# Kernel optimization log

Hardware: AMD Instinct MI355X
Metric: run time of the kernel (lower is better)

## Reference

```python
import jax, jax.numpy as jnp
import numpy as np

D = 1024
HS = 64
NH = D // HS
NEG_INF = -1e30


def setup_inputs() -> dict:
    key = jax.random.key(0)
    ks = jax.random.split(key, 8)
    B, S = 4, 2048
    x = jax.random.normal(ks[0], (B, S, D), dtype=jnp.float32)
    y = jax.random.normal(ks[1], (B, S, D), dtype=jnp.float32)
    pad_mask = jnp.ones((B, S), dtype=jnp.int32)
    time_attention = jnp.ones((S, S), dtype=jnp.int32)
    scale = 1.0 / np.sqrt(D)
    Wq = jax.random.normal(ks[2], (D, D), dtype=jnp.float32) * scale
    Wk = jax.random.normal(ks[3], (D, D), dtype=jnp.float32) * scale
    Wv = jax.random.normal(ks[4], (D, D), dtype=jnp.float32) * scale
    Wp = jax.random.normal(ks[5], (D, D), dtype=jnp.float32) * scale
    bp = jnp.zeros((D,), dtype=jnp.float32)
    return {"x": x, "y": y, "pad_mask": pad_mask, "time_attention": time_attention,
            "Wq": Wq, "Wk": Wk, "Wv": Wv, "Wp": Wp, "bp": bp}


def reference(x, y, pad_mask, time_attention, Wq, Wk, Wv, Wp, bp):
    B, S, _ = x.shape
    Sy = y.shape[1]
    # q/k/v projections (Linear: x @ W.T), split into heads -> [B, H, S, hs]
    q = (y @ Wq.T).reshape(B, Sy, NH, HS).transpose(0, 2, 1, 3)
    k = (x @ Wk.T).reshape(B, S, NH, HS).transpose(0, 2, 1, 3)
    v = (x @ Wv.T).reshape(B, S, NH, HS).transpose(0, 2, 1, 3)
    # scaled scores [B, H, Sy, S]
    att = jnp.einsum('bhqe,bhke->bhqk', q, k) * (HS ** -0.5)
    # causal mask (tril[:S, :S])
    causal = jnp.tril(jnp.ones((S, S), dtype=jnp.bool_))
    att = jnp.where(causal[None, None, :Sy, :], att, NEG_INF)
    # pad mask over kv positions
    att = jnp.where(pad_mask[:, None, None, :] != 0, att, NEG_INF)
    # time attention mask [Sq, Sk]
    att = jnp.where(time_attention[None, None, :Sy, :] != 0, att, NEG_INF)
    p = jax.nn.softmax(att, axis=-1)  # dropout p=0 -> identity
    out = jnp.einsum('bhqk,bhke->bhqe', p, v)
    out = out.transpose(0, 2, 1, 3).reshape(B, Sy, D)
    return out @ Wp.T + bp
```

## Files before the change

kernel.cpp:

```cpp
#include <hip/hip_runtime.h>
#include <hip/hip_bf16.h>
#include <stdint.h>
#include <stddef.h>


typedef __attribute__((ext_vector_type(4))) float f32x4;
typedef __attribute__((ext_vector_type(8))) short s16x8;
typedef __attribute__((ext_vector_type(4))) float float4v;
typedef __attribute__((ext_vector_type(4))) int i32x4;
typedef __attribute__((ext_vector_type(2))) unsigned int u32x2;

#define DEV __device__ __forceinline__

constexpr int Bsz = 4, Sseq = 2048, Dm = 1024, NHn = 16, HSn = 64;
constexpr float QSCALE = 0.125f * 1.4426950408889634f;

constexpr size_t SZ_BF_XY = (size_t)Bsz * Sseq * Dm * 2;
constexpr size_t SZ_W     = (size_t)Dm * Dm * 2;
constexpr size_t OFF_XBF  = 0;
constexpr size_t OFF_YBF  = OFF_XBF + SZ_BF_XY;
constexpr size_t OFF_WQ   = OFF_YBF + SZ_BF_XY;
constexpr size_t OFF_WK   = OFF_WQ + SZ_W;
constexpr size_t OFF_WV   = OFF_WK + SZ_W;
constexpr size_t OFF_WP   = OFF_WV + SZ_W;
constexpr size_t OFF_QWS  = OFF_WP + SZ_W;
constexpr size_t OFF_KWS  = OFF_QWS + SZ_BF_XY;
constexpr size_t OFF_VTWS = OFF_KWS + SZ_BF_XY;
constexpr size_t OFF_OWS  = OFF_VTWS + SZ_BF_XY;
constexpr size_t OFF_FLAG = OFF_OWS + SZ_BF_XY;

DEV unsigned short f2bf(float f) {
  union { float f; unsigned int u; } v; v.f = f;
  unsigned int r = (v.u + 0x7FFFu + ((v.u >> 16) & 1u)) >> 16;
  return (unsigned short)r;
}

DEV void gll16(const void* g, void* l) {
  __builtin_amdgcn_global_load_lds((const __attribute__((address_space(1))) unsigned int*)g,
                                   (__attribute__((address_space(3))) unsigned int*)l, 16, 0, 0);
}

DEV unsigned int cvtpk(float a, float b) {
  unsigned int r;
  asm("v_cvt_pk_bf16_f32 %0, %1, %2" : "=v"(r) : "v"(a), "v"(b));
  return r;
}

__global__ void cvt_all(const float* __restrict__ x, const float* __restrict__ y,
                        const float* __restrict__ Wq, const float* __restrict__ Wk,
                        const float* __restrict__ Wv, const float* __restrict__ Wp,
                        const int* __restrict__ pad, const int* __restrict__ tmask,
                        char* __restrict__ ws, int* __restrict__ flags) {
  const int blk = blockIdx.x;
  if (blk >= 10240) {
    int bad = 0;
    if (blk < 10248) {
      const i32x4 v = ((const i32x4*)pad)[(blk - 10240) * 256 + threadIdx.x];
      bad = (v[0] == 0) | (v[1] == 0) | (v[2] == 0) | (v[3] == 0);
    } else {
      const i32x4* tp = (const i32x4*)tmask + ((size_t)(blk - 10248) * 256 + threadIdx.x) * 2;
      i32x4 v0 = tp[0], v1 = tp[1];
      bad = (v0[0] == 0) | (v0[1] == 0) | (v0[2] == 0) | (v0[3] == 0) |
            (v1[0] == 0) | (v1[1] == 0) | (v1[2] == 0) | (v1[3] == 0);
    }
    if (__builtin_amdgcn_ballot_w64(bad) != 0 && (threadIdx.x & 63) == 0)
      atomicOr(flags, 1);
    return;
  }
  const float* src;
  unsigned short* dst;
  int b8;
  float scale = 1.f;
  if (blk < 4096)      { src = x;  dst = (unsigned short*)(ws + OFF_XBF); b8 = blk; }
  else if (blk < 8192) { src = y;  dst = (unsigned short*)(ws + OFF_YBF); b8 = blk - 4096; }
  else if (blk < 8704) { src = Wq; dst = (unsigned short*)(ws + OFF_WQ);  b8 = blk - 8192; scale = QSCALE; }
  else if (blk < 9216) { src = Wk; dst = (unsigned short*)(ws + OFF_WK);  b8 = blk - 8704; }
  else if (blk < 9728) { src = Wv; dst = (unsigned short*)(ws + OFF_WV);  b8 = blk - 9216; }
  else                 { src = Wp; dst = (unsigned short*)(ws + OFF_WP);  b8 = blk - 9728; }
  const size_t i = (size_t)b8 * 256 + threadIdx.x;
  const float4v* s = (const float4v*)src + i * 2;
  float4v a = s[0], b = s[1];
  s16x8 o;
  o[0] = (short)f2bf(a[0] * scale); o[1] = (short)f2bf(a[1] * scale);
  o[2] = (short)f2bf(a[2] * scale); o[3] = (short)f2bf(a[3] * scale);
  o[4] = (short)f2bf(b[0] * scale); o[5] = (short)f2bf(b[1] * scale);
  o[6] = (short)f2bf(b[2] * scale); o[7] = (short)f2bf(b[3] * scale);
  *(s16x8*)(dst + i * 8) = o;
}

__global__ __launch_bounds__(256) void q_gemm(const unsigned short* __restrict__ A,
                                              const unsigned short* __restrict__ W,
                                              unsigned short* __restrict__ outb) {
  constexpr int K = 1024;
  __shared__ unsigned short sm[8192];
  unsigned short* lA = sm;
  unsigned short* lB = sm + 4096;
  const int tid = threadIdx.x;
  const int w = tid >> 6, lane = tid & 63, lo = lane & 15, hi = lane >> 4;
  const int wm = w >> 1, wn = w & 1;
  const int m0 = blockIdx.x * 128, n0 = blockIdx.y * 128;
  f32x4 acc[4][4] = {};

  for (int k0 = 0; k0 < K; k0 += 32) {
#pragma unroll
    for (int h = 0; h < 2; ++h) {
      int c = w * 64 + h * 256 + lane;
      gll16(A + (size_t)(m0 + (c >> 2)) * K + k0 + (c & 3) * 8, lA + (size_t)(w * 64 + h * 256) * 8);
      gll16(W + (size_t)(n0 + (c >> 2)) * K + k0 + (c & 3) * 8, lB + (size_t)(w * 64 + h * 256) * 8);
    }
    __syncthreads();
    s16x8 af[4], bfr[4];
#pragma unroll
    for (int mi = 0; mi < 4; ++mi) af[mi] = *(const s16x8*)&lA[(wm * 64 + mi * 16 + lo) * 32 + hi * 8];
#pragma unroll
    for (int ni = 0; ni < 4; ++ni) bfr[ni] = *(const s16x8*)&lB[(wn * 64 + ni * 16 + lo) * 32 + hi * 8];
#pragma unroll
    for (int mi = 0; mi < 4; ++mi)
#pragma unroll
      for (int ni = 0; ni < 4; ++ni)
        acc[mi][ni] = __builtin_amdgcn_mfma_f32_16x16x32_bf16(af[mi], bfr[ni], acc[mi][ni], 0, 0, 0);
    __syncthreads();
  }
#pragma unroll
  for (int mi = 0; mi < 4; ++mi)
#pragma unroll
    for (int ni = 0; ni < 4; ++ni)
#pragma unroll
      for (int j = 0; j < 4; ++j) {
        int m = m0 + wm * 64 + mi * 16 + hi * 4 + j;
        int n = n0 + wn * 64 + ni * 16 + lo;
        int b = m >> 11, s = m & 2047, hh = n >> 6, e = n & 63;
        outb[((size_t)(b * NHn + hh) * Sseq + s) * HSn + e] = f2bf(acc[mi][ni][j]);
      }
}

__global__ __launch_bounds__(256, 2) void kv_gemm(const unsigned short* __restrict__ A,
                                                  const unsigned short* __restrict__ Wk,
                                                  const unsigned short* __restrict__ Wv,
                                                  unsigned short* __restrict__ kws,
                                                  unsigned short* __restrict__ vtw) {
  constexpr int K = 1024;
  __shared__ unsigned short sm[17408];
  unsigned short* lA = sm;
  unsigned short* lBk = sm + 4096;
  unsigned short* lBv = sm + 8192;
  const int tid = threadIdx.x;
  const int w = tid >> 6, lane = tid & 63, lo = lane & 15, hi = lane >> 4;
  const int wm = w >> 1, wn = w & 1;
  const int m0 = blockIdx.x * 128, n0 = blockIdx.y * 128;
  f32x4 acck[4][4] = {}, accv[4][4] = {};

  for (int k0 = 0; k0 < K; k0 += 32) {
#pragma unroll
    for (int h = 0; h < 2; ++h) {
      int c = w * 64 + h * 256 + lane;
      size_t roff = (size_t)(c >> 2) * K + k0 + (c & 3) * 8;
      size_t loff = (size_t)(w * 64 + h * 256) * 8;
      gll16(A + (size_t)m0 * K + roff, lA + loff);
      gll16(Wk + (size_t)n0 * K + roff, lBk + loff);
      gll16(Wv + (size_t)n0 * K + roff, lBv + loff);
    }
    __syncthreads();
    s16x8 af[4], bfk[4], bfv[4];
#pragma unroll
    for (int mi = 0; mi < 4; ++mi) af[mi] = *(const s16x8*)&lA[(wm * 64 + mi * 16 + lo) * 32 + hi * 8];
#pragma unroll
    for (int ni = 0; ni < 4; ++ni) {
      bfk[ni] = *(const s16x8*)&lBk[(wn * 64 + ni * 16 + lo) * 32 + hi * 8];
      bfv[ni] = *(const s16x8*)&lBv[(wn * 64 + ni * 16 + lo) * 32 + hi * 8];
    }
#pragma unroll
    for (int mi = 0; mi < 4; ++mi)
#pragma unroll
      for (int ni = 0; ni < 4; ++ni) {
        acck[mi][ni] = __builtin_amdgcn_mfma_f32_16x16x32_bf16(af[mi], bfk[ni], acck[mi][ni], 0, 0, 0);
        accv[mi][ni] = __builtin_amdgcn_mfma_f32_16x16x32_bf16(af[mi], bfv[ni], accv[mi][ni], 0, 0, 0);
      }
    __syncthreads();
  }

#pragma unroll
  for (int mi = 0; mi < 4; ++mi)
#pragma unroll
    for (int ni = 0; ni < 4; ++ni)
#pragma unroll
      for (int j = 0; j < 4; ++j) {
        int m = m0 + wm * 64 + mi * 16 + hi * 4 + j;
        int n = n0 + wn * 64 + ni * 16 + lo;
        int b = m >> 11, s = m & 2047, hh = n >> 6, e = n & 63;
        kws[((size_t)(b * NHn + hh) * Sseq + s) * HSn + e] = f2bf(acck[mi][ni][j]);
      }
  __syncthreads();
#pragma unroll
  for (int mi = 0; mi < 4; ++mi)
#pragma unroll
    for (int ni = 0; ni < 4; ++ni)
#pragma unroll
      for (int j = 0; j < 4; ++j) {
        int ml = wm * 64 + mi * 16 + hi * 4 + j;
        int nl = wn * 64 + ni * 16 + lo;
        sm[(size_t)nl * 136 + ml] = f2bf(accv[mi][ni][j]);
      }
  __syncthreads();
  int nl = tid >> 1, half = tid & 1;
  int b = m0 >> 11, hh = (n0 + nl) >> 6, e = (n0 + nl) & 63;
  unsigned short* dst = vtw + ((size_t)(b * NHn + hh) * HSn + e) * Sseq + (m0 & 2047) + half * 64;
#pragma unroll
  for (int i = 0; i < 8; ++i)
    *(s16x8*)(dst + i * 8) = *(const s16x8*)&sm[(size_t)nl * 136 + half * 64 + i * 8];
}

__global__ __launch_bounds__(256) void gemm_p(const unsigned short* __restrict__ A,
                                              const unsigned short* __restrict__ W,
                                              float* __restrict__ outf,
                                              const float* __restrict__ bias) {
  constexpr int K = 1024;
  __shared__ unsigned short sm[8192];
  unsigned short* lA = sm;
  unsigned short* lB = sm + 4096;
  const int tid = threadIdx.x;
  const int w = tid >> 6, lane = tid & 63, lo = lane & 15, hi = lane >> 4;
  const int wm = w >> 1, wn = w & 1;
  const int m0 = blockIdx.x * 128, n0 = blockIdx.y * 128;
  f32x4 acc[4][4] = {};
  for (int k0 = 0; k0 < K; k0 += 32) {
#pragma unroll
    for (int h = 0; h < 2; ++h) {
      int c = w * 64 + h * 256 + lane;
      gll16(A + (size_t)(m0 + (c >> 2)) * K + k0 + (c & 3) * 8, lA + (size_t)(w * 64 + h * 256) * 8);
      gll16(W + (size_t)(n0 + (c >> 2)) * K + k0 + (c & 3) * 8, lB + (size_t)(w * 64 + h * 256) * 8);
    }
    __syncthreads();
    s16x8 af[4], bfr[4];
#pragma unroll
    for (int mi = 0; mi < 4; ++mi) af[mi] = *(const s16x8*)&lA[(wm * 64 + mi * 16 + lo) * 32 + hi * 8];
#pragma unroll
    for (int ni = 0; ni < 4; ++ni) bfr[ni] = *(const s16x8*)&lB[(wn * 64 + ni * 16 + lo) * 32 + hi * 8];
#pragma unroll
    for (int mi = 0; mi < 4; ++mi)
#pragma unroll
      for (int ni = 0; ni < 4; ++ni)
        acc[mi][ni] = __builtin_amdgcn_mfma_f32_16x16x32_bf16(af[mi], bfr[ni], acc[mi][ni], 0, 0, 0);
    __syncthreads();
  }
  float bv[4];
#pragma unroll
  for (int ni = 0; ni < 4; ++ni) bv[ni] = bias[n0 + wn * 64 + ni * 16 + lo];
#pragma unroll
  for (int mi = 0; mi < 4; ++mi)
#pragma unroll
    for (int ni = 0; ni < 4; ++ni)
#pragma unroll
      for (int j = 0; j < 4; ++j) {
        int m = m0 + wm * 64 + mi * 16 + hi * 4 + j;
        int n = n0 + wn * 64 + ni * 16 + lo;
        outf[(size_t)m * 1024 + n] = acc[mi][ni][j] + bv[ni];
      }
}

DEV void attn_unit16(const unsigned short* __restrict__ kbc,
                     const unsigned short* __restrict__ vbc,
                     const s16x8 (&qf)[2], f32x4 (&oacc)[4], f32x4& lacc,
                     float& mrun, const s16x8& ones,
                     unsigned short* __restrict__ pbw,
                     int k0, int qw0, int lo, int hi, int b,
                     const int* __restrict__ pad, const int* __restrict__ tmask,
                     bool trivial) {
  if (k0 > qw0 + 15) return;

  f32x4 st[4];
#pragma unroll
  for (int t = 0; t < 4; ++t) {
    f32x4 z = {0.f, 0.f, 0.f, 0.f};
#pragma unroll
    for (int kk = 0; kk < 2; ++kk) {
      s16x8 kfr = *(const s16x8*)&kbc[(t * 16 + lo) * 72 + kk * 32 + hi * 8];
      z = __builtin_amdgcn_mfma_f32_16x16x32_bf16(kfr, qf[kk], z, 0, 0, 0);
    }
    st[t] = z;
  }
  const int qg = qw0 + lo;
  if (k0 + 63 > qw0) {
#pragma unroll
    for (int t = 0; t < 4; ++t)
#pragma unroll
      for (int j = 0; j < 4; ++j)
        if (k0 + t * 16 + hi * 4 + j > qg) st[t][j] = -3e38f;
  }
  if (!trivial) {
#pragma unroll
    for (int t = 0; t < 4; ++t)
#pragma unroll
      for (int j = 0; j < 4; ++j) {
        int kg = k0 + t * 16 + hi * 4 + j;
        if (!pad[b * Sseq + kg] || !tmask[(size_t)qg * Sseq + kg]) st[t][j] = -3e38f;
      }
  }
  float m0v = fmaxf(fmaxf(st[0][0], st[0][1]), fmaxf(st[0][2], st[0][3]));
  float m1v = fmaxf(fmaxf(st[1][0], st[1][1]), fmaxf(st[1][2], st[1][3]));
  float m2v = fmaxf(fmaxf(st[2][0], st[2][1]), fmaxf(st[2][2], st[2][3]));
  float m3v = fmaxf(fmaxf(st[3][0], st[3][1]), fmaxf(st[3][2], st[3][3]));
  float mx = fmaxf(fmaxf(m0v, m1v), fmaxf(m2v, m3v));
  mx = fmaxf(mx, __shfl_xor(mx, 16, 64));
  mx = fmaxf(mx, __shfl_xor(mx, 32, 64));
  if (!__all(mx <= mrun + 11.f)) {
    const float mnew = fmaxf(mrun, mx);
    const float al = __builtin_amdgcn_exp2f(mrun - mnew);
    mrun = mnew;
#pragma unroll
    for (int et = 0; et < 4; ++et) oacc[et] *= al;
    lacc *= al;
  }
#pragma unroll
  for (int t = 0; t < 4; ++t)
#pragma unroll
    for (int j = 0; j < 4; ++j)
      st[t][j] = __builtin_amdgcn_exp2f(st[t][j] - mrun);
#pragma unroll
  for (int t = 0; t < 4; ++t) {
    u32x2 dd = {cvtpk(st[t][0], st[t][1]), cvtpk(st[t][2], st[t][3])};
    *(u32x2*)&pbw[lo * 72 + t * 16 + hi * 4] = dd;
  }
  s16x8 pf[2];
#pragma unroll
  for (int kk = 0; kk < 2; ++kk)
    pf[kk] = *(const s16x8*)&pbw[lo * 72 + kk * 32 + hi * 8];
#pragma unroll
  for (int et = 0; et < 4; ++et)
#pragma unroll
    for (int kk = 0; kk < 2; ++kk) {
      s16x8 vfr = *(const s16x8*)&vbc[(et * 16 + lo) * 72 + kk * 32 + hi * 8];
      oacc[et] = __builtin_amdgcn_mfma_f32_16x16x32_bf16(vfr, pf[kk], oacc[et], 0, 0, 0);
    }
  lacc = __builtin_amdgcn_mfma_f32_16x16x32_bf16(ones, pf[0], lacc, 0, 0, 0);
  lacc = __builtin_amdgcn_mfma_f32_16x16x32_bf16(ones, pf[1], lacc, 0, 0, 0);
}

DEV void attn_epi16(f32x4 (&oacc)[4], float lrun,
                    unsigned short* __restrict__ pbw,
                    unsigned short* __restrict__ O, int b, int hh, int qw0,
                    int lane, int lo, int hi) {
  const float inv = 1.f / lrun;
#pragma unroll
  for (int et = 0; et < 4; ++et) {
    f32x4 o = oacc[et] * inv;
    u32x2 d = {cvtpk(o[0], o[1]), cvtpk(o[2], o[3])};
    *(u32x2*)&pbw[lo * 72 + et * 16 + hi * 4] = d;
  }
  int q = lane >> 2, seg = lane & 3;
  unsigned short* dst = O + ((size_t)b * Sseq + qw0 + q) * Dm + hh * HSn + seg * 16;
  *(s16x8*)dst = *(const s16x8*)&pbw[q * 72 + seg * 16];
  *(s16x8*)(dst + 8) = *(const s16x8*)&pbw[q * 72 + seg * 16 + 8];
}

__global__ __launch_bounds__(512, 4) void attn_kernel(const unsigned short* __restrict__ Q,
                                                      const unsigned short* __restrict__ Kg,
                                                      const unsigned short* __restrict__ Vt,
                                                      unsigned short* __restrict__ O,
                                                      const int* __restrict__ pad,
                                                      const int* __restrict__ tmask,
                                                      const int* __restrict__ flags) {
  __shared__ unsigned short kb[2][64 * 72];
  __shared__ unsigned short vb[2][64 * 72];
  __shared__ unsigned short pb[8][16 * 72];

  const int ip = blockIdx.x, bh = blockIdx.y;
  const int b = bh >> 4, hh = bh & 15;
  const int tid = threadIdx.x, w = tid >> 6, lane = tid & 63, lo = lane & 15, hi = lane >> 4;
  const int qtA = ip, qtB = 15 - ip;
  const int qw0A = qtA * 128 + w * 16, qw0B = qtB * 128 + w * 16;
  const int ktA = 2 * qtA + 1;
  const int ktmax = 2 * qtB + 2;
  const bool trivial = flags[0] == 0;

  const unsigned short* Qb = Q + (size_t)bh * Sseq * HSn;
  const unsigned short* Kb = Kg + (size_t)bh * Sseq * HSn;
  const unsigned short* Vb = Vt + (size_t)bh * HSn * Sseq;

  s16x8 qfA[2], qfB[2];
#pragma unroll
  for (int kk = 0; kk < 2; ++kk) {
    qfA[kk] = *(const s16x8*)&Qb[(size_t)(qw0A + lo) * HSn + kk * 32 + hi * 8];
    qfB[kk] = *(const s16x8*)&Qb[(size_t)(qw0B + lo) * HSn + kk * 32 + hi * 8];
  }

  s16x8 ones;
#pragma unroll
  for (int j = 0; j < 8; ++j) ones[j] = (short)0x3F80;

  f32x4 oaccA[4] = {}, oaccB[4] = {};
  f32x4 laccA = {}, laccB = {};
  float mrunA = -3e38f, mrunB = -3e38f;

  const int shalf = tid >> 8, st_t = tid & 255;
  const int sr = st_t >> 2, sc = (st_t & 3) * 16;

  s16x8 r0, r1;
  if (shalf == 0) {
    const unsigned short* gk = Kb + (size_t)sr * HSn + sc;
    r0 = *(const s16x8*)gk; r1 = *(const s16x8*)(gk + 8);
    *(s16x8*)&kb[0][sr * 72 + sc] = r0; *(s16x8*)&kb[0][sr * 72 + sc + 8] = r1;
  } else {
    const unsigned short* gv = Vb + (size_t)sr * Sseq + sc;
    r0 = *(const s16x8*)gv; r1 = *(const s16x8*)(gv + 8);
    *(s16x8*)&vb[0][sr * 72 + sc] = r0; *(s16x8*)&vb[0][sr * 72 + sc + 8] = r1;
  }
  __syncthreads();

  for (int kt = 0; kt < ktmax; ++kt) {
    const int cur = kt & 1, k0 = kt * 64;
    const bool pre = (kt + 1 < ktmax);
    if (pre) {
      const int k1 = k0 + 64;
      if (shalf == 0) {
        const unsigned short* gk = Kb + (size_t)(k1 + sr) * HSn + sc;
        r0 = *(const s16x8*)gk; r1 = *(const s16x8*)(gk + 8);
      } else {
        const unsigned short* gv = Vb + (size_t)sr * Sseq + k1 + sc;
        r0 = *(const s16x8*)gv; r1 = *(const s16x8*)(gv + 8);
      }
    }
    const unsigned short* kbc = kb[cur];
    const unsigned short* vbc = vb[cur];
    if (kt <= ktA)
      attn_unit16(kbc, vbc, qfA, oaccA, laccA, mrunA, ones, pb[w],
                  k0, qw0A, lo, hi, b, pad, tmask, trivial);
    attn_unit16(kbc, vbc, qfB, oaccB, laccB, mrunB, ones, pb[w],
                k0, qw0B, lo, hi, b, pad, tmask, trivial);
    if (pre) {
      const int nb = cur ^ 1;
      if (shalf == 0) {
        *(s16x8*)&kb[nb][sr * 72 + sc] = r0; *(s16x8*)&kb[nb][sr * 72 + sc + 8] = r1;
      } else {
        *(s16x8*)&vb[nb][sr * 72 + sc] = r0; *(s16x8*)&vb[nb][sr * 72 + sc + 8] = r1;
      }
    }
    __syncthreads();
  }

  attn_epi16(oaccA, laccA[0], pb[w], O, b, hh, qw0A, lane, lo, hi);
  attn_epi16(oaccB, laccB[0], pb[w], O, b, hh, qw0B, lane, lo, hi);
}

extern "C" void kernel_launch(void* const* d_in, const int* in_sizes, int n_in,
                              void* d_out, int out_size, void* d_ws, size_t ws_size,
                              hipStream_t stream) {
  const float* x = (const float*)d_in[0];
  const float* y = (const float*)d_in[1];
  const int* pad = (const int*)d_in[2];
  const int* tmask = (const int*)d_in[3];
  const float* Wq = (const float*)d_in[4];
  const float* Wk = (const float*)d_in[5];
  const float* Wv = (const float*)d_in[6];
  const float* Wp = (const float*)d_in[7];
  const float* bp = (const float*)d_in[8];

  char* ws = (char*)d_ws;
  unsigned short* xbf = (unsigned short*)(ws + OFF_XBF);
  unsigned short* ybf = (unsigned short*)(ws + OFF_YBF);
  unsigned short* wqb = (unsigned short*)(ws + OFF_WQ);
  unsigned short* wkb = (unsigned short*)(ws + OFF_WK);
  unsigned short* wvb = (unsigned short*)(ws + OFF_WV);
  unsigned short* wpb = (unsigned short*)(ws + OFF_WP);
  unsigned short* qws = (unsigned short*)(ws + OFF_QWS);
  unsigned short* kws = (unsigned short*)(ws + OFF_KWS);
  unsigned short* vtw = (unsigned short*)(ws + OFF_VTWS);
  unsigned short* ows = (unsigned short*)(ws + OFF_OWS);
  int* flags = (int*)(ws + OFF_FLAG);

  hipMemsetAsync(flags, 0, 4, stream);
  cvt_all<<<12296, 256, 0, stream>>>(x, y, Wq, Wk, Wv, Wp, pad, tmask, ws, flags);

  q_gemm<<<dim3(64, 8), 256, 0, stream>>>(ybf, wqb, qws);
  kv_gemm<<<dim3(64, 8), 256, 0, stream>>>(xbf, wkb, wvb, kws, vtw);

  attn_kernel<<<dim3(8, 64), 512, 0, stream>>>(qws, kws, vtw, ows, pad, tmask, flags);

  gemm_p<<<dim3(64, 8), 256, 0, stream>>>(ows, wpb, (float*)d_out, bp);
}
```

Measured before the change: 192.8 us.

## Double-buffer GEMM LDS tiles and interleave attention A/B query units

The three projection GEMMs now use two LDS buffers. The loads for the next K-slice are issued before computing on the current one, so each iteration keeps one barrier instead of two and loads overlap with compute. In the attention kernel the two query tiles (A and B) are processed together per KV tile, so each K and V fragment is read from LDS once for both. This also gives the scheduler independent MFMA chains to interleave, and each warp gets separate P buffers for the two tiles. The costs are more LDS per block, which may lower occupancy, and a reliance on async LDS loads being complete at the single barrier.

```diff
diff --git a/kernel.cpp b/kernel.cpp
--- a/kernel.cpp
+++ b/kernel.cpp
@@ -92,23 +92,28 @@
                                               const unsigned short* __restrict__ W,
                                               unsigned short* __restrict__ outb) {
   constexpr int K = 1024;
-  __shared__ unsigned short sm[8192];
-  unsigned short* lA = sm;
-  unsigned short* lB = sm + 4096;
+  __shared__ unsigned short sm[2][8192];
   const int tid = threadIdx.x;
   const int w = tid >> 6, lane = tid & 63, lo = lane & 15, hi = lane >> 4;
   const int wm = w >> 1, wn = w & 1;
   const int m0 = blockIdx.x * 128, n0 = blockIdx.y * 128;
   f32x4 acc[4][4] = {};
 
-  for (int k0 = 0; k0 < K; k0 += 32) {
+  auto stage = [&](int buf, int k0) {
 #pragma unroll
     for (int h = 0; h < 2; ++h) {
       int c = w * 64 + h * 256 + lane;
-      gll16(A + (size_t)(m0 + (c >> 2)) * K + k0 + (c & 3) * 8, lA + (size_t)(w * 64 + h * 256) * 8);
-      gll16(W + (size_t)(n0 + (c >> 2)) * K + k0 + (c & 3) * 8, lB + (size_t)(w * 64 + h * 256) * 8);
-    }
-    __syncthreads();
+      gll16(A + (size_t)(m0 + (c >> 2)) * K + k0 + (c & 3) * 8, &sm[buf][0] + (size_t)(w * 64 + h * 256) * 8);
+      gll16(W + (size_t)(n0 + (c >> 2)) * K + k0 + (c & 3) * 8, &sm[buf][4096] + (size_t)(w * 64 + h * 256) * 8);
+    }
+  };
+
+  stage(0, 0);
+  __syncthreads();
+  for (int t = 0; t < 32; ++t) {
+    if (t < 31) stage((t + 1) & 1, (t + 1) * 32);
+    const unsigned short* lA = &sm[t & 1][0];
+    const unsigned short* lB = &sm[t & 1][4096];
     s16x8 af[4], bfr[4];
 #pragma unroll
     for (int mi = 0; mi < 4; ++mi) af[mi] = *(const s16x8*)&lA[(wm * 64 + mi * 16 + lo) * 32 + hi * 8];
@@ -140,27 +145,32 @@
                                                   unsigned short* __restrict__ kws,
                                                   unsigned short* __restrict__ vtw) {
   constexpr int K = 1024;
-  __shared__ unsigned short sm[17408];
-  unsigned short* lA = sm;
-  unsigned short* lBk = sm + 4096;
-  unsigned short* lBv = sm + 8192;
+  __shared__ unsigned short sm[2][12288];
   const int tid = threadIdx.x;
   const int w = tid >> 6, lane = tid & 63, lo = lane & 15, hi = lane >> 4;
   const int wm = w >> 1, wn = w & 1;
   const int m0 = blockIdx.x * 128, n0 = blockIdx.y * 128;
   f32x4 acck[4][4] = {}, accv[4][4] = {};
 
-  for (int k0 = 0; k0 < K; k0 += 32) {
+  auto stage = [&](int buf, int k0) {
 #pragma unroll
     for (int h = 0; h < 2; ++h) {
       int c = w * 64 + h * 256 + lane;
       size_t roff = (size_t)(c >> 2) * K + k0 + (c & 3) * 8;
       size_t loff = (size_t)(w * 64 + h * 256) * 8;
-      gll16(A + (size_t)m0 * K + roff, lA + loff);
-      gll16(Wk + (size_t)n0 * K + roff, lBk + loff);
-      gll16(Wv + (size_t)n0 * K + roff, lBv + loff);
-    }
-    __syncthreads();
+      gll16(A + (size_t)m0 * K + roff, &sm[buf][0] + loff);
+      gll16(Wk + (size_t)n0 * K + roff, &sm[buf][4096] + loff);
+      gll16(Wv + (size_t)n0 * K + roff, &sm[buf][8192] + loff);
+    }
+  };
+
+  stage(0, 0);
+  __syncthreads();
+  for (int t = 0; t < 32; ++t) {
+    if (t < 31) stage((t + 1) & 1, (t + 1) * 32);
+    const unsigned short* lA = &sm[t & 1][0];
+    const unsigned short* lBk = &sm[t & 1][4096];
+    const unsigned short* lBv = &sm[t & 1][8192];
     s16x8 af[4], bfk[4], bfv[4];
 #pragma unroll
     for (int mi = 0; mi < 4; ++mi) af[mi] = *(const s16x8*)&lA[(wm * 64 + mi * 16 + lo) * 32 + hi * 8];
@@ -190,6 +200,7 @@
         int b = m >> 11, s = m & 2047, hh = n >> 6, e = n & 63;
         kws[((size_t)(b * NHn + hh) * Sseq + s) * HSn + e] = f2bf(acck[mi][ni][j]);
       }
+  unsigned short* tp = &sm[0][0];
   __syncthreads();
 #pragma unroll
   for (int mi = 0; mi < 4; ++mi)
@@ -199,7 +210,7 @@
       for (int j = 0; j < 4; ++j) {
         int ml = wm * 64 + mi * 16 + hi * 4 + j;
         int nl = wn * 64 + ni * 16 + lo;
-        sm[(size_t)nl * 136 + ml] = f2bf(accv[mi][ni][j]);
+        tp[(size_t)nl * 136 + ml] = f2bf(accv[mi][ni][j]);
       }
   __syncthreads();
   int nl = tid >> 1, half = tid & 1;
@@ -207,7 +218,7 @@
   unsigned short* dst = vtw + ((size_t)(b * NHn + hh) * HSn + e) * Sseq + (m0 & 2047) + half * 64;
 #pragma unroll
   for (int i = 0; i < 8; ++i)
-    *(s16x8*)(dst + i * 8) = *(const s16x8*)&sm[(size_t)nl * 136 + half * 64 + i * 8];
+    *(s16x8*)(dst + i * 8) = *(const s16x8*)&tp[(size_t)nl * 136 + half * 64 + i * 8];
 }
 
 __global__ __launch_bounds__(256) void gemm_p(const unsigned short* __restrict__ A,
@@ -215,22 +226,28 @@
                                               float* __restrict__ outf,
                                               const float* __restrict__ bias) {
   constexpr int K = 1024;
-  __shared__ unsigned short sm[8192];
-  unsigned short* lA = sm;
-  unsigned short* lB = sm + 4096;
+  __shared__ unsigned short sm[2][8192];
   const int tid = threadIdx.x;
   const int w = tid >> 6, lane = tid & 63, lo = lane & 15, hi = lane >> 4;
   const int wm = w >> 1, wn = w & 1;
   const int m0 = blockIdx.x * 128, n0 = blockIdx.y * 128;
   f32x4 acc[4][4] = {};
-  for (int k0 = 0; k0 < K; k0 += 32) {
+
+  auto stage = [&](int buf, int k0) {
 #pragma unroll
     for (int h = 0; h < 2; ++h) {
       int c = w * 64 + h * 256 + lane;
-      gll16(A + (size_t)(m0 + (c >> 2)) * K + k0 + (c & 3) * 8, lA + (size_t)(w * 64 + h * 256) * 8);
-      gll16(W + (size_t)(n0 + (c >> 2)) * K + k0 + (c & 3) * 8, lB + (size_t)(w * 64 + h * 256) * 8);
-    }
-    __syncthreads();
+      gll16(A + (size_t)(m0 + (c >> 2)) * K + k0 + (c & 3) * 8, &sm[buf][0] + (size_t)(w * 64 + h * 256) * 8);
+      gll16(W + (size_t)(n0 + (c >> 2)) * K + k0 + (c & 3) * 8, &sm[buf][4096] + (size_t)(w * 64 + h * 256) * 8);
+    }
+  };
+
+  stage(0, 0);
+  __syncthreads();
+  for (int t = 0; t < 32; ++t) {
+    if (t < 31) stage((t + 1) & 1, (t + 1) * 32);
+    const unsigned short* lA = &sm[t & 1][0];
+    const unsigned short* lB = &sm[t & 1][4096];
     s16x8 af[4], bfr[4];
 #pragma unroll
     for (int mi = 0; mi < 4; ++mi) af[mi] = *(const s16x8*)&lA[(wm * 64 + mi * 16 + lo) * 32 + hi * 8];
@@ -258,27 +275,10 @@
       }
 }
 
-DEV void attn_unit16(const unsigned short* __restrict__ kbc,
-                     const unsigned short* __restrict__ vbc,
-                     const s16x8 (&qf)[2], f32x4 (&oacc)[4], f32x4& lacc,
-                     float& mrun, const s16x8& ones,
-                     unsigned short* __restrict__ pbw,
-                     int k0, int qw0, int lo, int hi, int b,
+DEV void softmax_col(f32x4 (&st)[4], int k0, int qw0, int lo, int hi, int b,
                      const int* __restrict__ pad, const int* __restrict__ tmask,
-                     bool trivial) {
-  if (k0 > qw0 + 15) return;
-
-  f32x4 st[4];
-#pragma unroll
-  for (int t = 0; t < 4; ++t) {
-    f32x4 z = {0.f, 0.f, 0.f, 0.f};
-#pragma unroll
-    for (int kk = 0; kk < 2; ++kk) {
-      s16x8 kfr = *(const s16x8*)&kbc[(t * 16 + lo) * 72 + kk * 32 + hi * 8];
-      z = __builtin_amdgcn_mfma_f32_16x16x32_bf16(kfr, qf[kk], z, 0, 0, 0);
-    }
-    st[t] = z;
-  }
+                     bool trivial, float& mrun, f32x4 (&oacc)[4], f32x4& lacc,
+                     unsigned short* __restrict__ pbw) {
   const int qg = qw0 + lo;
   if (k0 + 63 > qw0) {
 #pragma unroll
@@ -321,19 +321,6 @@
     u32x2 dd = {cvtpk(st[t][0], st[t][1]), cvtpk(st[t][2], st[t][3])};
     *(u32x2*)&pbw[lo * 72 + t * 16 + hi * 4] = dd;
   }
-  s16x8 pf[2];
-#pragma unroll
-  for (int kk = 0; kk < 2; ++kk)
-    pf[kk] = *(const s16x8*)&pbw[lo * 72 + kk * 32 + hi * 8];
-#pragma unroll
-  for (int et = 0; et < 4; ++et)
-#pragma unroll
-    for (int kk = 0; kk < 2; ++kk) {
-      s16x8 vfr = *(const s16x8*)&vbc[(et * 16 + lo) * 72 + kk * 32 + hi * 8];
-      oacc[et] = __builtin_amdgcn_mfma_f32_16x16x32_bf16(vfr, pf[kk], oacc[et], 0, 0, 0);
-    }
-  lacc = __builtin_amdgcn_mfma_f32_16x16x32_bf16(ones, pf[0], lacc, 0, 0, 0);
-  lacc = __builtin_amdgcn_mfma_f32_16x16x32_bf16(ones, pf[1], lacc, 0, 0, 0);
 }
 
 DEV void attn_epi16(f32x4 (&oacc)[4], float lrun,
@@ -362,14 +349,13 @@
                                                       const int* __restrict__ flags) {
   __shared__ unsigned short kb[2][64 * 72];
   __shared__ unsigned short vb[2][64 * 72];
-  __shared__ unsigned short pb[8][16 * 72];
+  __shared__ unsigned short pb[8][2][16 * 72];
 
   const int ip = blockIdx.x, bh = blockIdx.y;
   const int b = bh >> 4, hh = bh & 15;
   const int tid = threadIdx.x, w = tid >> 6, lane = tid & 63, lo = lane & 15, hi = lane >> 4;
   const int qtA = ip, qtB = 15 - ip;
   const int qw0A = qtA * 128 + w * 16, qw0B = qtB * 128 + w * 16;
-  const int ktA = 2 * qtA + 1;
   const int ktmax = 2 * qtB + 2;
   const bool trivial = flags[0] == 0;
 
@@ -422,11 +408,45 @@
     }
     const unsigned short* kbc = kb[cur];
     const unsigned short* vbc = vb[cur];
-    if (kt <= ktA)
-      attn_unit16(kbc, vbc, qfA, oaccA, laccA, mrunA, ones, pb[w],
-                  k0, qw0A, lo, hi, b, pad, tmask, trivial);
-    attn_unit16(kbc, vbc, qfB, oaccB, laccB, mrunB, ones, pb[w],
-                k0, qw0B, lo, hi, b, pad, tmask, trivial);
+    const bool actB = (k0 <= qw0B + 15);
+    if (actB) {
+      const bool actA = (k0 <= qw0A + 15);
+      f32x4 stA[4], stB[4];
+#pragma unroll
+      for (int t = 0; t < 4; ++t) {
+        f32x4 zA = {0.f, 0.f, 0.f, 0.f}, zB = {0.f, 0.f, 0.f, 0.f};
+#pragma unroll
+        for (int kk = 0; kk < 2; ++kk) {
+          s16x8 kfr = *(const s16x8*)&kbc[(t * 16 + lo) * 72 + kk * 32 + hi * 8];
+          if (actA) zA = __builtin_amdgcn_mfma_f32_16x16x32_bf16(kfr, qfA[kk], zA, 0, 0, 0);
+          zB = __builtin_amdgcn_mfma_f32_16x16x32_bf16(kfr, qfB[kk], zB, 0, 0, 0);
+        }
+        stA[t] = zA; stB[t] = zB;
+      }
+      if (actA)
+        softmax_col(stA, k0, qw0A, lo, hi, b, pad, tmask, trivial, mrunA, oaccA, laccA, pb[w][0]);
+      softmax_col(stB, k0, qw0B, lo, hi, b, pad, tmask, trivial, mrunB, oaccB, laccB, pb[w][1]);
+      s16x8 pfA[2], pfB[2];
+#pragma unroll
+      for (int kk = 0; kk < 2; ++kk) {
+        if (actA) pfA[kk] = *(const s16x8*)&pb[w][0][lo * 72 + kk * 32 + hi * 8];
+        pfB[kk] = *(const s16x8*)&pb[w][1][lo * 72 + kk * 32 + hi * 8];
+      }
+#pragma unroll
+      for (int et = 0; et < 4; ++et)
+#pragma unroll
+        for (int kk = 0; kk < 2; ++kk) {
+          s16x8 vfr = *(const s16x8*)&vbc[(et * 16 + lo) * 72 + kk * 32 + hi * 8];
+          if (actA) oaccA[et] = __builtin_amdgcn_mfma_f32_16x16x32_bf16(vfr, pfA[kk], oaccA[et], 0, 0, 0);
+          oaccB[et] = __builtin_amdgcn_mfma_f32_16x16x32_bf16(vfr, pfB[kk], oaccB[et], 0, 0, 0);
+        }
+      if (actA) {
+        laccA = __builtin_amdgcn_mfma_f32_16x16x32_bf16(ones, pfA[0], laccA, 0, 0, 0);
+        laccA = __builtin_amdgcn_mfma_f32_16x16x32_bf16(ones, pfA[1], laccA, 0, 0, 0);
+      }
+      laccB = __builtin_amdgcn_mfma_f32_16x16x32_bf16(ones, pfB[0], laccB, 0, 0, 0);
+      laccB = __builtin_amdgcn_mfma_f32_16x16x32_bf16(ones, pfB[1], laccB, 0, 0, 0);
+    }
     if (pre) {
       const int nb = cur ^ 1;
       if (shalf == 0) {
@@ -438,8 +458,8 @@
     __syncthreads();
   }
 
-  attn_epi16(oaccA, laccA[0], pb[w], O, b, hh, qw0A, lane, lo, hi);
-  attn_epi16(oaccB, laccB[0], pb[w], O, b, hh, qw0B, lane, lo, hi);
+  attn_epi16(oaccA, laccA[0], pb[w][0], O, b, hh, qw0A, lane, lo, hi);
+  attn_epi16(oaccB, laccB[0], pb[w][1], O, b, hh, qw0B, lane, lo, hi);
 }
 
 extern "C" void kernel_launch(void* const* d_in, const int* in_sizes, int n_in,
```

After: 212.6 us, median of 2. 1.1x slower.

## Double-buffer LDS tiles in projection GEMMs and swap attention grid order

Applied to the files above, without the earlier changes.

The three projection GEMMs now keep two LDS stages and issue the global-to-LDS loads for the next K-slice before computing on the current one, so memory latency can overlap with MFMA work. The attention launch swaps grid axes so that neighbouring blocks cover different heads and batches rather than query tiles of the same head, which changes dispatch order and load balance. The cost is double the LDS footprint per GEMM block, which can lower occupancy, especially in kv_gemm. The loop body visible here has no barrier between issuing the next stage and reading the current one, so correctness depends on the unseen tail of the loop keeping its trailing sync.

```diff
diff --git a/kernel.cpp b/kernel.cpp
--- a/kernel.cpp
+++ b/kernel.cpp
@@ -92,23 +92,28 @@
                                               const unsigned short* __restrict__ W,
                                               unsigned short* __restrict__ outb) {
   constexpr int K = 1024;
-  __shared__ unsigned short sm[8192];
-  unsigned short* lA = sm;
-  unsigned short* lB = sm + 4096;
+  __shared__ unsigned short sm[2][8192];
   const int tid = threadIdx.x;
   const int w = tid >> 6, lane = tid & 63, lo = lane & 15, hi = lane >> 4;
   const int wm = w >> 1, wn = w & 1;
   const int m0 = blockIdx.x * 128, n0 = blockIdx.y * 128;
   f32x4 acc[4][4] = {};
 
-  for (int k0 = 0; k0 < K; k0 += 32) {
+  auto stage = [&](int buf, int k0) {
 #pragma unroll
     for (int h = 0; h < 2; ++h) {
       int c = w * 64 + h * 256 + lane;
-      gll16(A + (size_t)(m0 + (c >> 2)) * K + k0 + (c & 3) * 8, lA + (size_t)(w * 64 + h * 256) * 8);
-      gll16(W + (size_t)(n0 + (c >> 2)) * K + k0 + (c & 3) * 8, lB + (size_t)(w * 64 + h * 256) * 8);
-    }
-    __syncthreads();
+      gll16(A + (size_t)(m0 + (c >> 2)) * K + k0 + (c & 3) * 8, &sm[buf][0] + (size_t)(w * 64 + h * 256) * 8);
+      gll16(W + (size_t)(n0 + (c >> 2)) * K + k0 + (c & 3) * 8, &sm[buf][4096] + (size_t)(w * 64 + h * 256) * 8);
+    }
+  };
+
+  stage(0, 0);
+  __syncthreads();
+  for (int t = 0; t < 32; ++t) {
+    if (t < 31) stage((t + 1) & 1, (t + 1) * 32);
+    const unsigned short* lA = &sm[t & 1][0];
+    const unsigned short* lB = &sm[t & 1][4096];
     s16x8 af[4], bfr[4];
 #pragma unroll
     for (int mi = 0; mi < 4; ++mi) af[mi] = *(const s16x8*)&lA[(wm * 64 + mi * 16 + lo) * 32 + hi * 8];
@@ -140,27 +145,32 @@
                                                   unsigned short* __restrict__ kws,
                                                   unsigned short* __restrict__ vtw) {
   constexpr int K = 1024;
-  __shared__ unsigned short sm[17408];
-  unsigned short* lA = sm;
-  unsigned short* lBk = sm + 4096;
-  unsigned short* lBv = sm + 8192;
+  __shared__ unsigned short sm[2][12288];
   const int tid = threadIdx.x;
   const int w = tid >> 6, lane = tid & 63, lo = lane & 15, hi = lane >> 4;
   const int wm = w >> 1, wn = w & 1;
   const int m0 = blockIdx.x * 128, n0 = blockIdx.y * 128;
   f32x4 acck[4][4] = {}, accv[4][4] = {};
 
-  for (int k0 = 0; k0 < K; k0 += 32) {
+  auto stage = [&](int buf, int k0) {
 #pragma unroll
     for (int h = 0; h < 2; ++h) {
       int c = w * 64 + h * 256 + lane;
       size_t roff = (size_t)(c >> 2) * K + k0 + (c & 3) * 8;
       size_t loff = (size_t)(w * 64 + h * 256) * 8;
-      gll16(A + (size_t)m0 * K + roff, lA + loff);
-      gll16(Wk + (size_t)n0 * K + roff, lBk + loff);
-      gll16(Wv + (size_t)n0 * K + roff, lBv + loff);
-    }
-    __syncthreads();
+      gll16(A + (size_t)m0 * K + roff, &sm[buf][0] + loff);
+      gll16(Wk + (size_t)n0 * K + roff, &sm[buf][4096] + loff);
+      gll16(Wv + (size_t)n0 * K + roff, &sm[buf][8192] + loff);
+    }
+  };
+
+  stage(0, 0);
+  __syncthreads();
+  for (int t = 0; t < 32; ++t) {
+    if (t < 31) stage((t + 1) & 1, (t + 1) * 32);
+    const unsigned short* lA = &sm[t & 1][0];
+    const unsigned short* lBk = &sm[t & 1][4096];
+    const unsigned short* lBv = &sm[t & 1][8192];
     s16x8 af[4], bfk[4], bfv[4];
 #pragma unroll
     for (int mi = 0; mi < 4; ++mi) af[mi] = *(const s16x8*)&lA[(wm * 64 + mi * 16 + lo) * 32 + hi * 8];
@@ -190,6 +200,7 @@
         int b = m >> 11, s = m & 2047, hh = n >> 6, e = n & 63;
         kws[((size_t)(b * NHn + hh) * Sseq + s) * HSn + e] = f2bf(acck[mi][ni][j]);
       }
+  unsigned short* tp = &sm[0][0];
   __syncthreads();
 #pragma unroll
   for (int mi = 0; mi < 4; ++mi)
@@ -199,7 +210,7 @@
       for (int j = 0; j < 4; ++j) {
         int ml = wm * 64 + mi * 16 + hi * 4 + j;
         int nl = wn * 64 + ni * 16 + lo;
-        sm[(size_t)nl * 136 + ml] = f2bf(accv[mi][ni][j]);
+        tp[(size_t)nl * 136 + ml] = f2bf(accv[mi][ni][j]);
       }
   __syncthreads();
   int nl = tid >> 1, half = tid & 1;
@@ -207,7 +218,7 @@
   unsigned short* dst = vtw + ((size_t)(b * NHn + hh) * HSn + e) * Sseq + (m0 & 2047) + half * 64;
 #pragma unroll
   for (int i = 0; i < 8; ++i)
-    *(s16x8*)(dst + i * 8) = *(const s16x8*)&sm[(size_t)nl * 136 + half * 64 + i * 8];
+    *(s16x8*)(dst + i * 8) = *(const s16x8*)&tp[(size_t)nl * 136 + half * 64 + i * 8];
 }
 
 __global__ __launch_bounds__(256) void gemm_p(const unsigned short* __restrict__ A,
@@ -215,22 +226,28 @@
                                               float* __restrict__ outf,
                                               const float* __restrict__ bias) {
   constexpr int K = 1024;
-  __shared__ unsigned short sm[8192];
-  unsigned short* lA = sm;
-  unsigned short* lB = sm + 4096;
+  __shared__ unsigned short sm[2][8192];
   const int tid = threadIdx.x;
   const int w = tid >> 6, lane = tid & 63, lo = lane & 15, hi = lane >> 4;
   const int wm = w >> 1, wn = w & 1;
   const int m0 = blockIdx.x * 128, n0 = blockIdx.y * 128;
   f32x4 acc[4][4] = {};
-  for (int k0 = 0; k0 < K; k0 += 32) {
+
+  auto stage = [&](int buf, int k0) {
 #pragma unroll
     for (int h = 0; h < 2; ++h) {
       int c = w * 64 + h * 256 + lane;
-      gll16(A + (size_t)(m0 + (c >> 2)) * K + k0 + (c & 3) * 8, lA + (size_t)(w * 64 + h * 256) * 8);
-      gll16(W + (size_t)(n0 + (c >> 2)) * K + k0 + (c & 3) * 8, lB + (size_t)(w * 64 + h * 256) * 8);
-    }
-    __syncthreads();
+      gll16(A + (size_t)(m0 + (c >> 2)) * K + k0 + (c & 3) * 8, &sm[buf][0] + (size_t)(w * 64 + h * 256) * 8);
+      gll16(W + (size_t)(n0 + (c >> 2)) * K + k0 + (c & 3) * 8, &sm[buf][4096] + (size_t)(w * 64 + h * 256) * 8);
+    }
+  };
+
+  stage(0, 0);
+  __syncthreads();
+  for (int t = 0; t < 32; ++t) {
+    if (t < 31) stage((t + 1) & 1, (t + 1) * 32);
+    const unsigned short* lA = &sm[t & 1][0];
+    const unsigned short* lB = &sm[t & 1][4096];
     s16x8 af[4], bfr[4];
 #pragma unroll
     for (int mi = 0; mi < 4; ++mi) af[mi] = *(const s16x8*)&lA[(wm * 64 + mi * 16 + lo) * 32 + hi * 8];
@@ -364,7 +381,7 @@
   __shared__ unsigned short vb[2][64 * 72];
   __shared__ unsigned short pb[8][16 * 72];
 
-  const int ip = blockIdx.x, bh = blockIdx.y;
+  const int ip = blockIdx.y, bh = blockIdx.x;
   const int b = bh >> 4, hh = bh & 15;
   const int tid = threadIdx.x, w = tid >> 6, lane = tid & 63, lo = lane & 15, hi = lane >> 4;
   const int qtA = ip, qtB = 15 - ip;
@@ -474,7 +491,7 @@
   q_gemm<<<dim3(64, 8), 256, 0, stream>>>(ybf, wqb, qws);
   kv_gemm<<<dim3(64, 8), 256, 0, stream>>>(xbf, wkb, wvb, kws, vtw);
 
-  attn_kernel<<<dim3(8, 64), 512, 0, stream>>>(qws, kws, vtw, ows, pad, tmask, flags);
+  attn_kernel<<<dim3(64, 8), 512, 0, stream>>>(qws, kws, vtw, ows, pad, tmask, flags);
 
   gemm_p<<<dim3(64, 8), 256, 0, stream>>>(ows, wpb, (float*)d_out, bp);
 }
```

Result: no change. 190.8 us (-1.0%).
